# Kernel optimization log

Measured on AMD Instinct MI355X. Metric: run time of the kernel, lower is better.

## Reference

```python
import jax, jax.numpy as jnp
import numpy as np

C = 128      # channels
ALPHA = 0.5
B, LX, LY = 8, 128, 1024


def setup_inputs() -> dict:
    key = jax.random.key(0)
    ks = jax.random.split(key, 10)
    s = 1.0 / np.sqrt(C)
    sh = 1.0 / np.sqrt(C // 2)
    return {
        "x": jax.random.normal(ks[0], (B, C, LX), dtype=jnp.float32),
        "y": jax.random.normal(ks[1], (B, C, LY), dtype=jnp.float32),
        "W_drug": jax.random.uniform(ks[2], (C, C), jnp.float32, -s, s),
        "b_drug": jax.random.uniform(ks[3], (C,), jnp.float32, -s, s),
        "W_prot": jax.random.uniform(ks[4], (C, C), jnp.float32, -s, s),
        "b_prot": jax.random.uniform(ks[5], (C,), jnp.float32, -s, s),
        "W_down": jax.random.uniform(ks[6], (C, C // 2), jnp.float32, -s, s),
        "b_down": jax.random.uniform(ks[7], (C // 2,), jnp.float32, -s, s),
        "W_up": jax.random.uniform(ks[8], (C // 2, C), jnp.float32, -sh, sh),
        "b_up": jax.random.uniform(ks[9], (C,), jnp.float32, -sh, sh),
    }


def reference(x, y, W_drug, b_drug, W_prot, b_prot, W_down, b_down, W_up, b_up):
    # x: [B, C, Lx], y: [B, C, Ly]
    drug_att = jnp.einsum("bcl,cd->bld", x, W_drug) + b_drug      # [B, Lx, C]
    prot_att = jnp.einsum("bcl,cd->bld", y, W_prot) + b_prot      # [B, Ly, C]
    # broadcast-add -> [B, Lx, Ly, C]
    s = jax.nn.relu(drug_att[:, :, None, :] + prot_att[:, None, :, :])
    h = jax.nn.relu(jnp.einsum("bxyc,ch->bxyh", s, W_down) + b_down)  # [B,Lx,Ly,C/2]
    atten = jnp.einsum("bxyh,hc->bxyc", h, W_up) + b_up              # [B,Lx,Ly,C]
    comp = jnp.mean(atten, axis=2)   # [B, Lx, C]
    prot = jnp.mean(atten, axis=1)   # [B, Ly, C]
    comp_g = comp.transpose(0, 2, 1)  # [B, C, Lx]
    prot_g = prot.transpose(0, 2, 1)  # [B, C, Ly]
    comp_gate = jax.nn.sigmoid(comp_g) * jnp.tanh(comp_g)
    prot_gate = jax.nn.sigmoid(prot_g) * jnp.tanh(prot_g)
    drug_out = x * ALPHA + x * comp_gate
    prot_out = y * ALPHA + y * prot_gate
    return (drug_out, prot_out)
```

## Files before the change

kernel.cpp:

```cpp
#include <hip/hip_runtime.h>
#include <hip/hip_bf16.h>
#include <math.h>

#define B_  8
#define C_  128
#define CH_ 64
#define LX_ 128
#define LY_ 1024

typedef __attribute__((ext_vector_type(8)))  _Float16 half8;
typedef __attribute__((ext_vector_type(16))) float f32x16;

__global__ __launch_bounds__(128) void k1_att(
    const float* __restrict__ x, const float* __restrict__ y,
    const float* __restrict__ Wd, const float* __restrict__ bd,
    const float* __restrict__ Wp, const float* __restrict__ bp,
    const float* __restrict__ Wdown,
    _Float16* __restrict__ datt, _Float16* __restrict__ patt,
    _Float16* __restrict__ wdTh)
{
    const int blk = blockIdx.x;
    const int t = threadIdx.x;
    if (blk < 64) {
        int u = blk * 128 + t;
        wdTh[u] = (_Float16)Wdown[(u & 127) * CH_ + (u >> 7)];
    }
    const float* src; const float* W; const float* bias; _Float16* dst; int L;
    int b, l0;
    if (blk < 256) {
        int row0 = blk * 4; b = row0 >> 7; l0 = row0 & 127;
        src = x; W = Wd; bias = bd; dst = datt; L = LX_;
    } else {
        int row0 = (blk - 256) * 4; b = row0 >> 10; l0 = row0 & 1023;
        src = y; W = Wp; bias = bp; dst = patt; L = LY_;
    }
    __shared__ float col[128][8];
    {
        const float* sp = src + ((long)b * C_ + t) * L + l0;
        float4 v = *(const float4*)sp;
        *(float4*)&col[t][0] = v;
    }
    __syncthreads();
    float acc0 = bias[t], acc1 = acc0, acc2 = acc0, acc3 = acc0;
    #pragma unroll 8
    for (int c = 0; c < 128; ++c) {
        float w = W[c * 128 + t];
        float4 s = *(const float4*)&col[c][0];
        acc0 = fmaf(s.x, w, acc0); acc1 = fmaf(s.y, w, acc1);
        acc2 = fmaf(s.z, w, acc2); acc3 = fmaf(s.w, w, acc3);
    }
    _Float16* dp = dst + ((long)b * L + l0) * C_ + t;
    dp[0]      = (_Float16)acc0; dp[C_]     = (_Float16)acc1;
    dp[2 * C_] = (_Float16)acc2; dp[3 * C_] = (_Float16)acc3;
}

__global__ __launch_bounds__(256, 4) void k2_main(
    const _Float16* __restrict__ datt, const _Float16* __restrict__ patt,
    const _Float16* __restrict__ wdTh, const float* __restrict__ bdown,
    _Float16* __restrict__ HxPh, _Float16* __restrict__ HyPh)
{
    const int raw = blockIdx.x;
    const int bid = (raw & 7) * 128 + (raw >> 3);
    const int lyblk = bid & 31;
    const int lxblk = (bid >> 5) & 3;
    const int b     = bid >> 7;
    const int t   = threadIdx.x;
    const int w   = t >> 6;
    const int wk  = w >> 1;
    const int wl  = w & 1;
    const int l   = t & 63;
    const int h   = l >> 5;
    const int c32 = l & 31;

    __shared__ _Float16 dTh[32][136];
    __shared__ float compWp[32][2][66];

    {
        const _Float16* dsrc = datt + ((long)(b * LX_) + lxblk * 32) * C_;
        #pragma unroll
        for (int i = 0; i < 2; ++i) {
            int idx = t + i * 256;
            *(half8*)&dTh[idx >> 4][(idx & 15) * 8] = *(const half8*)(dsrc + idx * 8);
        }
    }

    const _Float16* prow = patt + ((long)(b * LY_) + lyblk * 32 + c32) * C_ + h * 8;
    const _Float16* wrow = wdTh + (wk * 32 + c32) * C_ + h * 8;
    half8 pv[8], bf[8];
    #pragma unroll
    for (int kt = 0; kt < 8; ++kt) {
        pv[kt] = *(const half8*)(prow + kt * 16);
        bf[kt] = *(const half8*)(wrow + kt * 16);
    }
    const float bdr = bdown[wk * 32 + c32];
    const half8 hz = {};
    __syncthreads();

    float hy[16];
    #pragma unroll
    for (int r = 0; r < 16; ++r) hy[r] = 0.f;

    #pragma unroll 1
    for (int r = 0; r < 16; ++r) {
        const _Float16* dp = &dTh[wl * 16 + r][h * 8];
        f32x16 acc = {};
        #pragma unroll
        for (int kt = 0; kt < 8; ++kt) {
            half8 d = *(const half8*)(dp + kt * 16);
            half8 s = __builtin_elementwise_max(d + pv[kt], hz);
            acc = __builtin_amdgcn_mfma_f32_32x32x16_f16(s, bf[kt], acc, 0, 0, 0);
        }
        float pa0 = 0.f, pa1 = 0.f, pa2 = 0.f, pa3 = 0.f;
        #pragma unroll
        for (int rr = 0; rr < 16; ++rr) {
            float v = fmaxf(acc[rr] + bdr, 0.f);
            hy[rr] += v;
            if      ((rr & 3) == 0) pa0 += v;
            else if ((rr & 3) == 1) pa1 += v;
            else if ((rr & 3) == 2) pa2 += v;
            else                    pa3 += v;
        }
        compWp[wl * 16 + r][h][wk * 32 + c32] = (pa0 + pa1) + (pa2 + pa3);
    }

    {
        _Float16* hyp = HyPh
            + (((long)(lxblk * 2 + wl) * B_ + b) * LY_ + lyblk * 32) * 64
            + wk * 32 + c32;
        #pragma unroll
        for (int rr = 0; rr < 16; ++rr) {
            int ly = (rr & 3) + 8 * (rr >> 2) + 4 * h;
            hyp[(long)ly * 64] = (_Float16)hy[rr];
        }
    }
    __syncthreads();

    {
        _Float16* hxp = HxPh + (((long)lyblk * B_ + b) * LX_ + lxblk * 32) * 64;
        for (int u = t; u < 2048; u += 256) {
            int r = u >> 6, c = u & 63;
            hxp[u] = (_Float16)(compWp[r][0][c] + compWp[r][1][c]);
        }
    }
}

__global__ __launch_bounds__(256) void k3_gate(
    const _Float16* __restrict__ HxPh, const _Float16* __restrict__ HyPh,
    const float* __restrict__ wup, const float* __restrict__ bup,
    const float* __restrict__ x, const float* __restrict__ y,
    float* __restrict__ out)
{
    const int b = blockIdx.y;
    const int t = threadIdx.x;
    const _Float16* part; const float* xin; float* outp; int L; float invN; int l0;
    int nq; long qstr;
    if (blockIdx.x < 4) {
        part = HxPh; nq = 32; qstr = (long)B_ * LX_ * 64;
        xin = x; outp = out; L = LX_; invN = 1.f / 1024.f; l0 = blockIdx.x * 32;
    } else {
        part = HyPh; nq = 8;  qstr = (long)B_ * LY_ * 64;
        xin = y; outp = out + (long)B_ * C_ * LX_; L = LY_; invN = 1.f / 128.f;
        l0 = (blockIdx.x - 4) * 32;
    }
    __shared__ float Ht[32][72];
    __shared__ float Wt[64][136];
    __shared__ float gg[32][133];

    const _Float16* p0 = part + ((long)b * L + l0) * 64;
    for (int u = t; u < 2048; u += 256) {
        float a0 = 0.f, a1 = 0.f, a2 = 0.f, a3 = 0.f;
        #pragma unroll 4
        for (int q = 0; q < nq; q += 4) {
            a0 += (float)p0[(long)q * qstr + u];
            a1 += (float)p0[(long)(q + 1) * qstr + u];
            a2 += (float)p0[(long)(q + 2) * qstr + u];
            a3 += (float)p0[(long)(q + 3) * qstr + u];
        }
        Ht[u >> 6][u & 63] = (a0 + a1) + (a2 + a3);
    }
    #pragma unroll
    for (int i = 0; i < 8; ++i) {
        int idx = t + i * 256;
        int r = idx >> 5, c4 = (idx & 31) * 4;
        *(float4*)&Wt[r][c4] = *(const float4*)(wup + idx * 4);
    }
    __syncthreads();

    const int lrow = t >> 3, cg = (t & 7) * 4;
    float acc[4][4];
    #pragma unroll
    for (int jj = 0; jj < 4; ++jj)
        #pragma unroll
        for (int i = 0; i < 4; ++i) acc[jj][i] = 0.f;
    #pragma unroll 4
    for (int k = 0; k < 64; ++k) {
        float hv = Ht[lrow][k];
        #pragma unroll
        for (int jj = 0; jj < 4; ++jj) {
            float4 wv = *(const float4*)&Wt[k][cg + 32 * jj];
            acc[jj][0] = fmaf(hv, wv.x, acc[jj][0]);
            acc[jj][1] = fmaf(hv, wv.y, acc[jj][1]);
            acc[jj][2] = fmaf(hv, wv.z, acc[jj][2]);
            acc[jj][3] = fmaf(hv, wv.w, acc[jj][3]);
        }
    }
    #pragma unroll
    for (int jj = 0; jj < 4; ++jj)
        #pragma unroll
        for (int i = 0; i < 4; ++i) {
            int c = cg + 32 * jj + i;
            float v = fmaf(acc[jj][i], invN, bup[c]);
            float sg = 1.f / (1.f + expf(-v));
            gg[lrow][c] = sg * tanhf(v);
        }
    __syncthreads();
    for (int u = t; u < 4096; u += 256) {
        int c = u >> 5, li = u & 31;
        long idx = ((long)b * C_ + c) * L + l0 + li;
        outp[idx] = xin[idx] * (0.5f + gg[li][c]);
    }
}

extern "C" void kernel_launch(void* const* d_in, const int* in_sizes, int n_in,
                              void* d_out, int out_size, void* d_ws, size_t ws_size,
                              hipStream_t stream) {
    (void)in_sizes; (void)n_in; (void)out_size; (void)ws_size;
    const float* x     = (const float*)d_in[0];
    const float* y     = (const float*)d_in[1];
    const float* Wdrug = (const float*)d_in[2];
    const float* bdrug = (const float*)d_in[3];
    const float* Wprot = (const float*)d_in[4];
    const float* bprot = (const float*)d_in[5];
    const float* Wdown = (const float*)d_in[6];
    const float* bdown = (const float*)d_in[7];
    const float* Wup   = (const float*)d_in[8];
    const float* bup   = (const float*)d_in[9];
    float* out = (float*)d_out;
    char* ws = (char*)d_ws;

    _Float16* datt = (_Float16*)ws;
    _Float16* patt = (_Float16*)(ws + 262144);
    _Float16* wdTh = (_Float16*)(ws + 2359296);
    _Float16* HxPh = (_Float16*)(ws + 2375680);
    _Float16* HyPh = (_Float16*)(ws + 6569984);

    hipLaunchKernelGGL(k1_att, dim3(2304), dim3(128), 0, stream,
                       x, y, Wdrug, bdrug, Wprot, bprot, Wdown, datt, patt, wdTh);
    hipLaunchKernelGGL(k2_main, dim3(1024), dim3(256), 0, stream,
                       datt, patt, wdTh, bdown, HxPh, HyPh);
    hipLaunchKernelGGL(k3_gate, dim3(36, 8), dim3(256), 0, stream,
                       HxPh, HyPh, Wup, bup, x, y, out);
}
```

Measured before the change: 62.97 us.

## Rewrite input projection kernel with fp16 MFMA over 32-row tiles

The first kernel, which projects x and y through W_drug/W_prot, now uses fp16 32x32x16 MFMA instructions instead of scalar FMA loops. Each 256-thread block handles 32 rows of one batch, on a 36x8 grid instead of 2304 small blocks. Inputs and the full weight matrix are staged transposed into shared memory as fp16. This aims to cut the FFMA cost, but every block reloads and converts the entire 128x128 weight matrix and does strided global reads, and fp16 rounding of the inputs adds precision loss.

Result: faster. 57.28 us (median of 2 runs) (-9.0%).

```diff
diff --git a/kernel.cpp b/kernel.cpp
--- a/kernel.cpp
+++ b/kernel.cpp
@@ -11,7 +11,7 @@
 typedef __attribute__((ext_vector_type(8)))  _Float16 half8;
 typedef __attribute__((ext_vector_type(16))) float f32x16;
 
-__global__ __launch_bounds__(128) void k1_att(
+__global__ __launch_bounds__(256) void k1_att(
     const float* __restrict__ x, const float* __restrict__ y,
     const float* __restrict__ Wd, const float* __restrict__ bd,
     const float* __restrict__ Wp, const float* __restrict__ bp,
@@ -19,39 +19,61 @@
     _Float16* __restrict__ datt, _Float16* __restrict__ patt,
     _Float16* __restrict__ wdTh)
 {
-    const int blk = blockIdx.x;
-    const int t = threadIdx.x;
-    if (blk < 64) {
-        int u = blk * 128 + t;
+    const int b  = blockIdx.y;
+    const int lt = blockIdx.x;
+    const int t  = threadIdx.x;
+    if (b == 0 && lt < 32) {
+        int u = lt * 256 + t;
         wdTh[u] = (_Float16)Wdown[(u & 127) * CH_ + (u >> 7)];
     }
-    const float* src; const float* W; const float* bias; _Float16* dst; int L;
-    int b, l0;
-    if (blk < 256) {
-        int row0 = blk * 4; b = row0 >> 7; l0 = row0 & 127;
-        src = x; W = Wd; bias = bd; dst = datt; L = LX_;
-    } else {
-        int row0 = (blk - 256) * 4; b = row0 >> 10; l0 = row0 & 1023;
-        src = y; W = Wp; bias = bp; dst = patt; L = LY_;
-    }
-    __shared__ float col[128][8];
-    {
-        const float* sp = src + ((long)b * C_ + t) * L + l0;
-        float4 v = *(const float4*)sp;
-        *(float4*)&col[t][0] = v;
-    }
-    __syncthreads();
-    float acc0 = bias[t], acc1 = acc0, acc2 = acc0, acc3 = acc0;
-    #pragma unroll 8
-    for (int c = 0; c < 128; ++c) {
-        float w = W[c * 128 + t];
-        float4 s = *(const float4*)&col[c][0];
-        acc0 = fmaf(s.x, w, acc0); acc1 = fmaf(s.y, w, acc1);
-        acc2 = fmaf(s.z, w, acc2); acc3 = fmaf(s.w, w, acc3);
-    }
-    _Float16* dp = dst + ((long)b * L + l0) * C_ + t;
-    dp[0]      = (_Float16)acc0; dp[C_]     = (_Float16)acc1;
-    dp[2 * C_] = (_Float16)acc2; dp[3 * C_] = (_Float16)acc3;
+    const float* src; const float* W; const float* bias; _Float16* dst; int L; int l0;
+    if (lt < 4) { src = x; W = Wd; bias = bd; dst = datt; L = LX_; l0 = lt * 32; }
+    else        { src = y; W = Wp; bias = bp; dst = patt; L = LY_; l0 = (lt - 4) * 32; }
+
+    __shared__ _Float16 At[32][136];
+    __shared__ _Float16 Wt[128][136];
+
+    {
+        const float* xsrc = src + (long)b * C_ * L + l0;
+        #pragma unroll
+        for (int i = 0; i < 16; ++i) {
+            int u = t + i * 256;
+            int c = u >> 5, lq = u & 31;
+            At[lq][c] = (_Float16)xsrc[(long)c * L + lq];
+        }
+        #pragma unroll
+        for (int i = 0; i < 64; ++i) {
+            int u = t + i * 256;
+            int c = u >> 7, d = u & 127;
+            Wt[d][c] = (_Float16)W[u];
+        }
+    }
+    __syncthreads();
+
+    const int w   = t >> 6;
+    const int l   = t & 63;
+    const int h   = l >> 5;
+    const int c32 = l & 31;
+    const int d0  = w * 32;
+
+    half8 af[8], bf[8];
+    #pragma unroll
+    for (int kt = 0; kt < 8; ++kt) {
+        af[kt] = *(const half8*)&At[c32][kt * 16 + h * 8];
+        bf[kt] = *(const half8*)&Wt[d0 + c32][kt * 16 + h * 8];
+    }
+    f32x16 acc = {};
+    #pragma unroll
+    for (int kt = 0; kt < 8; ++kt)
+        acc = __builtin_amdgcn_mfma_f32_32x32x16_f16(af[kt], bf[kt], acc, 0, 0, 0);
+
+    const float bv = bias[d0 + c32];
+    _Float16* dp = dst + ((long)b * L + l0) * C_ + d0 + c32;
+    #pragma unroll
+    for (int rr = 0; rr < 16; ++rr) {
+        int row = (rr & 3) + 8 * (rr >> 2) + 4 * h;
+        dp[(long)row * C_] = (_Float16)(acc[rr] + bv);
+    }
 }
 
 __global__ __launch_bounds__(256, 4) void k2_main(
@@ -244,7 +266,7 @@
     _Float16* HxPh = (_Float16*)(ws + 2375680);
     _Float16* HyPh = (_Float16*)(ws + 6569984);
 
-    hipLaunchKernelGGL(k1_att, dim3(2304), dim3(128), 0, stream,
+    hipLaunchKernelGGL(k1_att, dim3(36, 8), dim3(256), 0, stream,
                        x, y, Wdrug, bdrug, Wprot, bprot, Wdown, datt, patt, wdTh);
     hipLaunchKernelGGL(k2_main, dim3(1024), dim3(256), 0, stream,
                        datt, patt, wdTh, bdown, HxPh, HyPh);
```
